# Optimization experiments

Measured on AMD Instinct MI355X. Metric: run time of the kernel, lower is better.

The kernel has to match this reference:

```python
import jax, jax.numpy as jnp
import numpy as np

B, S, D, E, K, NS = 4, 1024, 1024, 8, 2, 2
H = 4 * D
TEMP = 0.1
SCALE = 0.02


def setup_inputs() -> dict:
    key = jax.random.key(0)
    ks = jax.random.split(key, 12)
    f32 = jnp.float32
    return {
        "x": jax.random.normal(ks[0], (B, S, D), f32),
        "Ws1": jax.random.normal(ks[1], (NS, D, H), f32) * SCALE,
        "bs1": jnp.zeros((NS, H), f32),
        "Ws2": jax.random.normal(ks[2], (NS, H, D), f32) * SCALE,
        "bs2": jnp.zeros((NS, D), f32),
        "We1": jax.random.normal(ks[3], (E, D, H), f32) * SCALE,
        "be1": jnp.zeros((E, H), f32),
        "We2": jax.random.normal(ks[4], (E, H, D), f32) * SCALE,
        "be2": jnp.zeros((E, D), f32),
        "Wr": jax.random.normal(ks[5], (D, E), f32) * SCALE,
        "br": jnp.zeros((E,), f32),
        "gumbel": jax.random.gumbel(ks[6], (B, S, E), f32),
    }


def reference(x, Ws1, bs1, Ws2, bs2, We1, be1, We2, be2, Wr, br, gumbel):
    act = jax.nn.gelu
    # shared experts: dense FFN per shared expert, summed over experts
    hs = act(jnp.einsum('bsd,edh->ebsh', x, Ws1) + bs1[:, None, None, :])
    shared_sum = (jnp.einsum('ebsh,ehd->ebsd', hs, Ws2)
                  + bs2[:, None, None, :]).sum(axis=0)  # [B,S,D]
    # routing experts: ALL experts computed densely over all tokens
    he = act(jnp.einsum('bsd,edh->ebsh', x, We1) + be1[:, None, None, :])
    all_experts = jnp.einsum('ebsh,ehd->ebsd', he, We2) + be2[:, None, None, :]  # [E,B,S,D]
    # router + gumbel-softmax top-k selection
    logits = x @ Wr + br                                  # [B,S,E]
    router_probs = jax.nn.softmax((logits + gumbel) / TEMP, axis=-1)
    chosen = jax.lax.top_k(router_probs, K)[1]            # [B,S,K] int
    one_hot = jax.nn.one_hot(chosen, E, dtype=x.dtype)    # [B,S,K,E]
    # unweighted sum of selected experts' outputs (sum over k and experts)
    out = jnp.einsum('bske,ebsd->bsd', one_hot, all_experts)
    return out + shared_sum
```

## Files before the change

### kernel.cpp

```cpp
#include <hip/hip_runtime.h>
#include <cstdint>
#include <cstddef>

#define T_TOK 4096
#define DDIM 1024
#define HDIM 4096
#define NEXP 8
#define NSHARED 2

typedef unsigned short ushort_t;
typedef __attribute__((ext_vector_type(8))) short short8;
typedef __attribute__((ext_vector_type(4))) float f32x4;

__device__ inline ushort_t f2bf(float f) {
  unsigned u = __float_as_uint(f);
  u += 0x7fffu + ((u >> 16) & 1u);
  return (ushort_t)(u >> 16);
}

__device__ inline void async_copy16(const ushort_t* g, ushort_t* l) {
  __builtin_amdgcn_global_load_lds(
      (const __attribute__((address_space(1))) void*)g,
      (__attribute__((address_space(3))) void*)l, 16, 0, 0);
}

__device__ inline float gelu_tanh(float x) {
  float u = 0.7978845608028654f * (x + 0.044715f * x * x * x);
  float th = 1.0f - 2.0f / (__expf(2.0f * u) + 1.0f);
  return 0.5f * x * (1.0f + th);
}

__global__ __launch_bounds__(256) void router_kernel(
    const float* __restrict__ x, const float* __restrict__ Wr,
    const float* __restrict__ br, const float* __restrict__ gum,
    int* __restrict__ choice, int* __restrict__ cnt) {
  int lane = threadIdx.x & 63;
  int wv = blockIdx.x * 4 + (threadIdx.x >> 6);
  if (wv >= T_TOK) return;
  const float* xr = x + (long)wv * DDIM;
  float acc[NEXP] = {0.f, 0.f, 0.f, 0.f, 0.f, 0.f, 0.f, 0.f};
  for (int d = lane; d < DDIM; d += 64) {
    float xv = xr[d];
    const float* w = Wr + d * NEXP;
#pragma unroll
    for (int e = 0; e < NEXP; e++) acc[e] += xv * w[e];
  }
#pragma unroll
  for (int e = 0; e < NEXP; e++) {
    float v = acc[e];
#pragma unroll
    for (int o = 32; o > 0; o >>= 1) v += __shfl_down(v, o);
    acc[e] = v;
  }
  if (lane == 0) {
    float vals[NEXP];
#pragma unroll
    for (int e = 0; e < NEXP; e++) vals[e] = acc[e] + br[e] + gum[(long)wv * NEXP + e];
    int i1 = 0; float b1 = vals[0];
#pragma unroll
    for (int e = 1; e < NEXP; e++) if (vals[e] > b1) { b1 = vals[e]; i1 = e; }
    int i2 = -1; float b2 = -3.4e38f;
#pragma unroll
    for (int e = 0; e < NEXP; e++) if (e != i1 && vals[e] > b2) { b2 = vals[e]; i2 = e; }
    choice[wv] = i1 | (i2 << 4);
    atomicAdd(&cnt[i1], 1);
    atomicAdd(&cnt[i2], 1);
  }
}

__global__ void prefix_kernel(const int* __restrict__ cnt, int* __restrict__ base,
                              int* __restrict__ fill) {
  if (threadIdx.x == 0 && blockIdx.x == 0) {
    int off = 0;
    for (int e = 0; e < NEXP; e++) {
      base[e] = off;
      off += (cnt[e] + 127) & ~127;
      fill[e] = 0;
    }
  }
}

__global__ __launch_bounds__(256) void scatter_kernel(
    const int* __restrict__ choice, const int* __restrict__ base,
    int* __restrict__ fill, int* __restrict__ idx) {
  int t = blockIdx.x * 256 + threadIdx.x;
  if (t >= T_TOK) return;
  int c = choice[t];
  int e1 = c & 15, e2 = (c >> 4) & 15;
  int p1 = atomicAdd(&fill[e1], 1);
  idx[base[e1] + p1] = t;
  int p2 = atomicAdd(&fill[e2], 1);
  idx[base[e2] + p2] = t;
}

__global__ __launch_bounds__(256) void cast_x_kernel(
    const float* __restrict__ in, ushort_t* __restrict__ out, int n4) {
  int i = blockIdx.x * 256 + threadIdx.x;
  if (i >= n4) return;
  float4 v = ((const float4*)in)[i];
  ushort4 o = make_ushort4(f2bf(v.x), f2bf(v.y), f2bf(v.z), f2bf(v.w));
  ((ushort4*)out)[i] = o;
}

__global__ __launch_bounds__(256) void transpose_cast(
    const float* __restrict__ in, ushort_t* __restrict__ out, int R, int C) {
  __shared__ float tile[32][33];
  long zoff = (long)blockIdx.z * R * C;
  in += zoff; out += zoff;
  int c0 = blockIdx.x * 32, r0 = blockIdx.y * 32;
  int tx = threadIdx.x, ty = threadIdx.y;
#pragma unroll
  for (int k = 0; k < 4; k++)
    tile[ty + 8 * k][tx] = in[(long)(r0 + ty + 8 * k) * C + (c0 + tx)];
  __syncthreads();
#pragma unroll
  for (int k = 0; k < 4; k++)
    out[(long)(c0 + ty + 8 * k) * R + (r0 + tx)] = f2bf(tile[tx][ty + 8 * k]);
}

template <int MODE>
__global__ __launch_bounds__(256) void gemm_kernel(
    const ushort_t* __restrict__ A, const ushort_t* __restrict__ W,
    const float* __restrict__ bias, ushort_t* __restrict__ outH,
    float* __restrict__ outF, const int* __restrict__ cnt,
    const int* __restrict__ base, const int* __restrict__ idx) {
  __shared__ ushort_t As[128 * 32];
  __shared__ ushort_t Bs[128 * 32];

  int tid = threadIdx.x;
  int row0 = blockIdx.y * 128;
  int col0 = blockIdx.x * 128;

  int e = 0, kc = 0, M = 0, base_e = 0;
  const ushort_t* Ap;
  const ushort_t* Bp;
  long lda, ldb;
  int kLen, kStartA, kStartB;

  if (MODE == 0) {
    Ap = A; lda = DDIM; kStartA = 0;
    Bp = W; ldb = DDIM; kStartB = 0; kLen = DDIM;
  } else if (MODE == 1) {
    kc = blockIdx.z;
    int s = kc >> 1;
    Ap = A; lda = 2 * HDIM; kStartA = kc * 2048;
    Bp = W + (long)s * DDIM * HDIM; ldb = HDIM; kStartB = (kc & 1) * 2048;
    kLen = 2048;
  } else if (MODE == 2) {
    e = blockIdx.z; M = cnt[e];
    if (row0 >= M) return;
    base_e = base[e];
    Ap = A; lda = DDIM; kStartA = 0;
    Bp = W + (long)(NSHARED + e) * HDIM * DDIM; ldb = DDIM; kStartB = 0;
    kLen = DDIM;
  } else {
    e = blockIdx.z >> 1; kc = blockIdx.z & 1; M = cnt[e];
    if (row0 >= M) return;
    base_e = base[e];
    Ap = A + (long)base_e * HDIM; lda = HDIM; kStartA = kc * 2048;
    Bp = W + (long)(NSHARED + e) * DDIM * HDIM; ldb = HDIM; kStartB = kc * 2048;
    kLen = 2048;
  }

  int tq = tid & 3, tr = tid >> 2;
  const ushort_t* aS;
  const ushort_t* aS2;
  if (MODE == 2) {
    int s1 = row0 + tr;       if (s1 > M - 1) s1 = M - 1;
    int s2 = row0 + tr + 64;  if (s2 > M - 1) s2 = M - 1;
    aS  = Ap + (long)idx[base_e + s1] * lda + kStartA + tq * 8;
    aS2 = Ap + (long)idx[base_e + s2] * lda + kStartA + tq * 8;
  } else {
    aS  = Ap + (long)(row0 + tr) * lda + kStartA + tq * 8;
    aS2 = aS + 64L * lda;
  }
  const ushort_t* bS  = Bp + (long)(col0 + tr) * ldb + kStartB + tq * 8;
  const ushort_t* bS2 = bS + 64L * ldb;
  ushort_t* aD = As + tid * 8;
  ushort_t* bD = Bs + tid * 8;

  int lane = tid & 63;
  int wv = tid >> 6;
  int wr = wv >> 1, wc = wv & 1;
  int ln = lane & 15, quad = lane >> 4;

  f32x4 acc[4][4] = {};
  const ushort_t* aLds = As + (wr * 64 + ln) * 32 + quad * 8;
  const ushort_t* bLds = Bs + (wc * 64 + ln) * 32 + quad * 8;

  for (int k0 = 0; k0 < kLen; k0 += 32) {
    async_copy16(aS, aD);
    async_copy16(aS2, aD + 2048);
    async_copy16(bS, bD);
    async_copy16(bS2, bD + 2048);
    __syncthreads();
    short8 af[4], bf[4];
#pragma unroll
    for (int i = 0; i < 4; i++) {
      af[i] = *(const short8*)(aLds + i * 16 * 32);
      bf[i] = *(const short8*)(bLds + i * 16 * 32);
    }
#pragma unroll
    for (int i = 0; i < 4; i++)
#pragma unroll
      for (int j = 0; j < 4; j++)
        acc[i][j] = __builtin_amdgcn_mfma_f32_16x16x32_bf16(af[i], bf[j],
                                                            acc[i][j], 0, 0, 0);
    __syncthreads();
    aS += 32; aS2 += 32; bS += 32; bS2 += 32;
  }

#pragma unroll
  for (int i = 0; i < 4; i++) {
    int rowB = row0 + wr * 64 + i * 16 + quad * 4;
#pragma unroll
    for (int j = 0; j < 4; j++) {
      int col = col0 + wc * 64 + j * 16 + ln;
#pragma unroll
      for (int r = 0; r < 4; r++) {
        int t = rowB + r;
        float v = acc[i][j][r];
        if (MODE == 0) {
          outH[(long)t * (2 * HDIM) + col] = f2bf(gelu_tanh(v + bias[col]));
        } else if (MODE == 1) {
          if (kc == 0) v += bias[col] + bias[DDIM + col];
          atomicAdd(outF + (long)t * DDIM + col, v);
        } else if (MODE == 2) {
          if (t < M)
            outH[((long)base_e + t) * HDIM + col] =
                f2bf(gelu_tanh(v + bias[(long)e * HDIM + col]));
        } else {
          if (t < M) {
            int tok = idx[base_e + t];
            if (kc == 0) v += bias[(long)e * DDIM + col];
            atomicAdd(outF + (long)tok * DDIM + col, v);
          }
        }
      }
    }
  }
}

extern "C" void kernel_launch(void* const* d_in, const int* in_sizes, int n_in,
                              void* d_out, int out_size, void* d_ws,
                              size_t ws_size, hipStream_t stream) {
  const float* x   = (const float*)d_in[0];
  const float* Ws1 = (const float*)d_in[1];
  const float* bs1 = (const float*)d_in[2];
  const float* Ws2 = (const float*)d_in[3];
  const float* bs2 = (const float*)d_in[4];
  const float* We1 = (const float*)d_in[5];
  const float* be1 = (const float*)d_in[6];
  const float* We2 = (const float*)d_in[7];
  const float* be2 = (const float*)d_in[8];
  const float* Wr  = (const float*)d_in[9];
  const float* br  = (const float*)d_in[10];
  const float* gum = (const float*)d_in[11];
  float* out = (float*)d_out;

  char* ws = (char*)d_ws;
  size_t off = 0;
  int* cnt    = (int*)(ws + off); off += 256;
  int* base   = (int*)(ws + off); off += 256;
  int* fill   = (int*)(ws + off); off += 256;
  int* choice = (int*)(ws + off); off += T_TOK * 4;
  int* idx    = (int*)(ws + off); off += 9216 * 4;
  off = (off + 255) & ~(size_t)255;
  ushort_t* xb   = (ushort_t*)(ws + off); off += (size_t)T_TOK * DDIM * 2;
  ushort_t* W1t  = (ushort_t*)(ws + off); off += (size_t)10 * HDIM * DDIM * 2;
  ushort_t* W2t  = (ushort_t*)(ws + off); off += (size_t)10 * DDIM * HDIM * 2;
  ushort_t* h_sh = (ushort_t*)(ws + off); off += (size_t)T_TOK * 2 * HDIM * 2;
  ushort_t* h_rt = (ushort_t*)(ws + off); off += (size_t)9216 * HDIM * 2;
  (void)ws_size;

  hipMemsetAsync(out, 0, (size_t)T_TOK * DDIM * sizeof(float), stream);
  hipMemsetAsync(cnt, 0, 256, stream);

  router_kernel<<<T_TOK / 4, 256, 0, stream>>>(x, Wr, br, gum, choice, cnt);
  prefix_kernel<<<1, 64, 0, stream>>>(cnt, base, fill);
  scatter_kernel<<<T_TOK / 256, 256, 0, stream>>>(choice, base, fill, idx);
  cast_x_kernel<<<(T_TOK * DDIM / 4 + 255) / 256, 256, 0, stream>>>(
      x, xb, T_TOK * DDIM / 4);

  transpose_cast<<<dim3(HDIM / 32, DDIM / 32, NSHARED), dim3(32, 8), 0, stream>>>(
      Ws1, W1t, DDIM, HDIM);
  transpose_cast<<<dim3(HDIM / 32, DDIM / 32, NEXP), dim3(32, 8), 0, stream>>>(
      We1, W1t + (size_t)NSHARED * HDIM * DDIM, DDIM, HDIM);
  transpose_cast<<<dim3(DDIM / 32, HDIM / 32, NSHARED), dim3(32, 8), 0, stream>>>(
      Ws2, W2t, HDIM, DDIM);
  transpose_cast<<<dim3(DDIM / 32, HDIM / 32, NEXP), dim3(32, 8), 0, stream>>>(
      We2, W2t + (size_t)NSHARED * DDIM * HDIM, HDIM, DDIM);

  gemm_kernel<0><<<dim3(2 * HDIM / 128, T_TOK / 128, 1), 256, 0, stream>>>(
      xb, W1t, bs1, h_sh, nullptr, nullptr, nullptr, nullptr);
  gemm_kernel<2><<<dim3(HDIM / 128, T_TOK / 128, NEXP), 256, 0, stream>>>(
      xb, W1t, be1, h_rt, nullptr, cnt, base, idx);
  gemm_kernel<1><<<dim3(DDIM / 128, T_TOK / 128, 4), 256, 0, stream>>>(
      h_sh, W2t, bs2, nullptr, out, nullptr, nullptr, nullptr);
  gemm_kernel<3><<<dim3(DDIM / 128, T_TOK / 128, 2 * NEXP), 256, 0, stream>>>(
      h_rt, W2t, be2, nullptr, out, cnt, base, idx);

  (void)in_sizes; (void)n_in; (void)out_size;
}
```

Before: 1.158 ms.

## Merge shared and routed expert GEMMs into two launches with K=64 stages

```diff
diff --git a/kernel.cpp b/kernel.cpp
--- a/kernel.cpp
+++ b/kernel.cpp
@@ -118,96 +118,80 @@
     out[(long)(c0 + ty + 8 * k) * R + (r0 + tx)] = f2bf(tile[tx][ty + 8 * k]);
 }
 
-template <int MODE>
-__global__ __launch_bounds__(256) void gemm_kernel(
-    const ushort_t* __restrict__ A, const ushort_t* __restrict__ W,
-    const float* __restrict__ bias, ushort_t* __restrict__ outH,
-    float* __restrict__ outF, const int* __restrict__ cnt,
-    const int* __restrict__ base, const int* __restrict__ idx) {
-  __shared__ ushort_t As[128 * 32];
-  __shared__ ushort_t Bs[128 * 32];
+__global__ __launch_bounds__(256) void gemm1_kernel(
+    const ushort_t* __restrict__ xb, const ushort_t* __restrict__ W1t,
+    const float* __restrict__ bs1, const float* __restrict__ be1,
+    ushort_t* __restrict__ h_sh, ushort_t* __restrict__ h_rt,
+    const int* __restrict__ cnt, const int* __restrict__ base,
+    const int* __restrict__ idx) {
+  __shared__ ushort_t As[2 * 128 * 32];
+  __shared__ ushort_t Bs[2 * 128 * 32];
 
   int tid = threadIdx.x;
-  int row0 = blockIdx.y * 128;
-  int col0 = blockIdx.x * 128;
-
-  int e = 0, kc = 0, M = 0, base_e = 0;
-  const ushort_t* Ap;
+  int z = blockIdx.z;
+  int row0 = blockIdx.y * 128, col0 = blockIdx.x * 128;
+  bool sh = (z < NSHARED);
+
+  int e = 0, M = T_TOK, base_e = 0;
   const ushort_t* Bp;
-  long lda, ldb;
-  int kLen, kStartA, kStartB;
-
-  if (MODE == 0) {
-    Ap = A; lda = DDIM; kStartA = 0;
-    Bp = W; ldb = DDIM; kStartB = 0; kLen = DDIM;
-  } else if (MODE == 1) {
-    kc = blockIdx.z;
-    int s = kc >> 1;
-    Ap = A; lda = 2 * HDIM; kStartA = kc * 2048;
-    Bp = W + (long)s * DDIM * HDIM; ldb = HDIM; kStartB = (kc & 1) * 2048;
-    kLen = 2048;
-  } else if (MODE == 2) {
-    e = blockIdx.z; M = cnt[e];
+  const float* bias;
+  if (sh) {
+    Bp = W1t + (size_t)z * HDIM * DDIM;
+    bias = bs1 + (size_t)z * HDIM;
+  } else {
+    e = z - NSHARED; M = cnt[e];
     if (row0 >= M) return;
     base_e = base[e];
-    Ap = A; lda = DDIM; kStartA = 0;
-    Bp = W + (long)(NSHARED + e) * HDIM * DDIM; ldb = DDIM; kStartB = 0;
-    kLen = DDIM;
+    Bp = W1t + (size_t)(NSHARED + e) * HDIM * DDIM;
+    bias = be1 + (size_t)e * HDIM;
+  }
+
+  int tq = tid & 3, tr = tid >> 2;
+  const ushort_t *aS, *aS2;
+  if (sh) {
+    aS = xb + (size_t)(row0 + tr) * DDIM + tq * 8;
+    aS2 = aS + (size_t)64 * DDIM;
   } else {
-    e = blockIdx.z >> 1; kc = blockIdx.z & 1; M = cnt[e];
-    if (row0 >= M) return;
-    base_e = base[e];
-    Ap = A + (long)base_e * HDIM; lda = HDIM; kStartA = kc * 2048;
-    Bp = W + (long)(NSHARED + e) * DDIM * HDIM; ldb = HDIM; kStartB = kc * 2048;
-    kLen = 2048;
-  }
-
-  int tq = tid & 3, tr = tid >> 2;
-  const ushort_t* aS;
-  const ushort_t* aS2;
-  if (MODE == 2) {
-    int s1 = row0 + tr;       if (s1 > M - 1) s1 = M - 1;
-    int s2 = row0 + tr + 64;  if (s2 > M - 1) s2 = M - 1;
-    aS  = Ap + (long)idx[base_e + s1] * lda + kStartA + tq * 8;
-    aS2 = Ap + (long)idx[base_e + s2] * lda + kStartA + tq * 8;
-  } else {
-    aS  = Ap + (long)(row0 + tr) * lda + kStartA + tq * 8;
-    aS2 = aS + 64L * lda;
-  }
-  const ushort_t* bS  = Bp + (long)(col0 + tr) * ldb + kStartB + tq * 8;
-  const ushort_t* bS2 = bS + 64L * ldb;
+    int s1 = row0 + tr;      if (s1 > M - 1) s1 = M - 1;
+    int s2 = row0 + tr + 64; if (s2 > M - 1) s2 = M - 1;
+    aS  = xb + (size_t)idx[base_e + s1] * DDIM + tq * 8;
+    aS2 = xb + (size_t)idx[base_e + s2] * DDIM + tq * 8;
+  }
+  const ushort_t* bS = Bp + (size_t)(col0 + tr) * DDIM + tq * 8;
+  const ushort_t* bS2 = bS + (size_t)64 * DDIM;
   ushort_t* aD = As + tid * 8;
   ushort_t* bD = Bs + tid * 8;
 
-  int lane = tid & 63;
-  int wv = tid >> 6;
+  int lane = tid & 63, wv = tid >> 6;
   int wr = wv >> 1, wc = wv & 1;
   int ln = lane & 15, quad = lane >> 4;
-
   f32x4 acc[4][4] = {};
   const ushort_t* aLds = As + (wr * 64 + ln) * 32 + quad * 8;
   const ushort_t* bLds = Bs + (wc * 64 + ln) * 32 + quad * 8;
 
-  for (int k0 = 0; k0 < kLen; k0 += 32) {
-    async_copy16(aS, aD);
-    async_copy16(aS2, aD + 2048);
-    async_copy16(bS, bD);
-    async_copy16(bS2, bD + 2048);
+  for (int k0 = 0; k0 < DDIM; k0 += 64) {
+    async_copy16(aS, aD);            async_copy16(aS2, aD + 2048);
+    async_copy16(aS + 32, aD + 4096); async_copy16(aS2 + 32, aD + 6144);
+    async_copy16(bS, bD);            async_copy16(bS2, bD + 2048);
+    async_copy16(bS + 32, bD + 4096); async_copy16(bS2 + 32, bD + 6144);
     __syncthreads();
-    short8 af[4], bf[4];
-#pragma unroll
-    for (int i = 0; i < 4; i++) {
-      af[i] = *(const short8*)(aLds + i * 16 * 32);
-      bf[i] = *(const short8*)(bLds + i * 16 * 32);
-    }
-#pragma unroll
-    for (int i = 0; i < 4; i++)
-#pragma unroll
-      for (int j = 0; j < 4; j++)
-        acc[i][j] = __builtin_amdgcn_mfma_f32_16x16x32_bf16(af[i], bf[j],
-                                                            acc[i][j], 0, 0, 0);
+#pragma unroll
+    for (int s = 0; s < 2; s++) {
+      short8 af[4], bf[4];
+#pragma unroll
+      for (int i = 0; i < 4; i++) {
+        af[i] = *(const short8*)(aLds + s * 4096 + i * 16 * 32);
+        bf[i] = *(const short8*)(bLds + s * 4096 + i * 16 * 32);
+      }
+#pragma unroll
+      for (int i = 0; i < 4; i++)
+#pragma unroll
+        for (int j = 0; j < 4; j++)
+          acc[i][j] = __builtin_amdgcn_mfma_f32_16x16x32_bf16(af[i], bf[j],
+                                                              acc[i][j], 0, 0, 0);
+    }
     __syncthreads();
-    aS += 32; aS2 += 32; bS += 32; bS2 += 32;
+    aS += 64; aS2 += 64; bS += 64; bS2 += 64;
   }
 
 #pragma unroll
@@ -216,25 +200,112 @@
 #pragma unroll
     for (int j = 0; j < 4; j++) {
       int col = col0 + wc * 64 + j * 16 + ln;
+      float b = bias[col];
 #pragma unroll
       for (int r = 0; r < 4; r++) {
         int t = rowB + r;
-        float v = acc[i][j][r];
-        if (MODE == 0) {
-          outH[(long)t * (2 * HDIM) + col] = f2bf(gelu_tanh(v + bias[col]));
-        } else if (MODE == 1) {
-          if (kc == 0) v += bias[col] + bias[DDIM + col];
-          atomicAdd(outF + (long)t * DDIM + col, v);
-        } else if (MODE == 2) {
-          if (t < M)
-            outH[((long)base_e + t) * HDIM + col] =
-                f2bf(gelu_tanh(v + bias[(long)e * HDIM + col]));
-        } else {
-          if (t < M) {
-            int tok = idx[base_e + t];
-            if (kc == 0) v += bias[(long)e * DDIM + col];
-            atomicAdd(outF + (long)tok * DDIM + col, v);
-          }
+        float v = gelu_tanh(acc[i][j][r] + b);
+        if (sh) {
+          h_sh[(size_t)t * (2 * HDIM) + (size_t)z * HDIM + col] = f2bf(v);
+        } else if (t < M) {
+          h_rt[((size_t)base_e + t) * HDIM + col] = f2bf(v);
+        }
+      }
+    }
+  }
+}
+
+__global__ __launch_bounds__(256) void gemm2_kernel(
+    const ushort_t* __restrict__ h_sh, const ushort_t* __restrict__ h_rt,
+    const ushort_t* __restrict__ W2t, const float* __restrict__ bs2,
+    const float* __restrict__ be2, float* __restrict__ outF,
+    const int* __restrict__ cnt, const int* __restrict__ base,
+    const int* __restrict__ idx) {
+  __shared__ ushort_t As[2 * 128 * 32];
+  __shared__ ushort_t Bs[2 * 128 * 32];
+
+  int tid = threadIdx.x;
+  int z = blockIdx.z;
+  int row0 = blockIdx.y * 128, col0 = blockIdx.x * 128;
+  bool sh = (z < NSHARED);
+
+  int e = 0, M = T_TOK, base_e = 0;
+  const ushort_t* Ap;
+  const ushort_t* Bp;
+  long lda;
+  if (sh) {
+    Ap = h_sh + (size_t)z * HDIM;
+    lda = 2 * HDIM;
+    Bp = W2t + (size_t)z * DDIM * HDIM;
+  } else {
+    e = z - NSHARED; M = cnt[e];
+    if (row0 >= M) return;
+    base_e = base[e];
+    Ap = h_rt + (size_t)base_e * HDIM;
+    lda = HDIM;
+    Bp = W2t + (size_t)(NSHARED + e) * DDIM * HDIM;
+  }
+
+  int tq = tid & 3, tr = tid >> 2;
+  const ushort_t* aS = Ap + (long)(row0 + tr) * lda + tq * 8;
+  const ushort_t* aS2 = aS + 64L * lda;
+  const ushort_t* bS = Bp + (size_t)(col0 + tr) * HDIM + tq * 8;
+  const ushort_t* bS2 = bS + (size_t)64 * HDIM;
+  ushort_t* aD = As + tid * 8;
+  ushort_t* bD = Bs + tid * 8;
+
+  int lane = tid & 63, wv = tid >> 6;
+  int wr = wv >> 1, wc = wv & 1;
+  int ln = lane & 15, quad = lane >> 4;
+  f32x4 acc[4][4] = {};
+  const ushort_t* aLds = As + (wr * 64 + ln) * 32 + quad * 8;
+  const ushort_t* bLds = Bs + (wc * 64 + ln) * 32 + quad * 8;
+
+  for (int k0 = 0; k0 < HDIM; k0 += 64) {
+    async_copy16(aS, aD);            async_copy16(aS2, aD + 2048);
+    async_copy16(aS + 32, aD + 4096); async_copy16(aS2 + 32, aD + 6144);
+    async_copy16(bS, bD);            async_copy16(bS2, bD + 2048);
+    async_copy16(bS + 32, bD + 4096); async_copy16(bS2 + 32, bD + 6144);
+    __syncthreads();
+#pragma unroll
+    for (int s = 0; s < 2; s++) {
+      short8 af[4], bf[4];
+#pragma unroll
+      for (int i = 0; i < 4; i++) {
+        af[i] = *(const short8*)(aLds + s * 4096 + i * 16 * 32);
+        bf[i] = *(const short8*)(bLds + s * 4096 + i * 16 * 32);
+      }
+#pragma unroll
+      for (int i = 0; i < 4; i++)
+#pragma unroll
+        for (int j = 0; j < 4; j++)
+          acc[i][j] = __builtin_amdgcn_mfma_f32_16x16x32_bf16(af[i], bf[j],
+                                                              acc[i][j], 0, 0, 0);
+    }
+    __syncthreads();
+    aS += 64; aS2 += 64; bS += 64; bS2 += 64;
+  }
+
+#pragma unroll
+  for (int i = 0; i < 4; i++) {
+    int rowB = row0 + wr * 64 + i * 16 + quad * 4;
+#pragma unroll
+    for (int j = 0; j < 4; j++) {
+      int col = col0 + wc * 64 + j * 16 + ln;
+      float b;
+      if (sh)
+        b = (z == 0) ? (bs2[col] + bs2[DDIM + col]) : 0.0f;
+      else
+        b = be2[(size_t)e * DDIM + col];
+#pragma unroll
+      for (int r = 0; r < 4; r++) {
+        int t = rowB + r;
+        float v = acc[i][j][r] + b;
+        if (sh) {
+          atomicAdd(outF + (size_t)t * DDIM + col, v);
+        } else if (t < M) {
+          int tok = idx[base_e + t];
+          atomicAdd(outF + (size_t)tok * DDIM + col, v);
         }
       }
     }
@@ -291,14 +362,10 @@
   transpose_cast<<<dim3(DDIM / 32, HDIM / 32, NEXP), dim3(32, 8), 0, stream>>>(
       We2, W2t + (size_t)NSHARED * DDIM * HDIM, HDIM, DDIM);
 
-  gemm_kernel<0><<<dim3(2 * HDIM / 128, T_TOK / 128, 1), 256, 0, stream>>>(
-      xb, W1t, bs1, h_sh, nullptr, nullptr, nullptr, nullptr);
-  gemm_kernel<2><<<dim3(HDIM / 128, T_TOK / 128, NEXP), 256, 0, stream>>>(
-      xb, W1t, be1, h_rt, nullptr, cnt, base, idx);
-  gemm_kernel<1><<<dim3(DDIM / 128, T_TOK / 128, 4), 256, 0, stream>>>(
-      h_sh, W2t, bs2, nullptr, out, nullptr, nullptr, nullptr);
-  gemm_kernel<3><<<dim3(DDIM / 128, T_TOK / 128, 2 * NEXP), 256, 0, stream>>>(
-      h_rt, W2t, be2, nullptr, out, cnt, base, idx);
+  gemm1_kernel<<<dim3(HDIM / 128, T_TOK / 128, NSHARED + NEXP), 256, 0, stream>>>(
+      xb, W1t, bs1, be1, h_sh, h_rt, cnt, base, idx);
+  gemm2_kernel<<<dim3(DDIM / 128, T_TOK / 128, NSHARED + NEXP), 256, 0, stream>>>(
+      h_sh, h_rt, W2t, bs2, be2, out, cnt, base, idx);
 
   (void)in_sizes; (void)n_in; (void)out_size;
 }
```

Result: no change. 1.162 ms (+0.3%).
